# Performance work log

Hardware: AMD Instinct MI355X
Metric: run time of the kernel (lower is better)

## Reference

```python
import jax, jax.numpy as jnp
import numpy as np

ALPHA = 0.01  # LeakyReLU negative slope

def _leaky(x):
    return jnp.where(x > 0, x, ALPHA * x)

def _conv(x, w, b):
    # x: NHWC, w: HWIO, valid padding, stride 1
    return jax.lax.conv_general_dilated(x, w, (1, 1), 'VALID',
        dimension_numbers=('NHWC', 'HWIO', 'NHWC')) + b

def _maxpool2(x):
    return jax.lax.reduce_window(x, -jnp.inf, jax.lax.max,
        (1, 2, 2, 1), (1, 2, 2, 1), 'VALID')

def setup_inputs() -> dict:
    key = jax.random.key(0)
    ks = jax.random.split(key, 32)
    B, S, H = 32, 197, 256
    FLAT = 47 * 62 * 64  # after conv/pool trunk = 186496
    def w(k, shape, fan_in):
        return jax.random.normal(k, shape, dtype=jnp.float32) * np.float32(1.0 / np.sqrt(fan_in))
    inp = {
        'x': jax.random.normal(ks[0], (B, S, H), dtype=jnp.float32),
        'conv1_w': w(ks[1], (3, 3, 1, 32), 9), 'conv1_b': jnp.zeros((32,), jnp.float32),
        'conv2_w': w(ks[2], (3, 3, 32, 64), 288), 'conv2_b': jnp.zeros((64,), jnp.float32),
        'w_c1': w(ks[3], (FLAT, 512), FLAT), 'b_c1': jnp.zeros((512,), jnp.float32),
        'w_c2': w(ks[4], (512, 256), 512), 'b_c2': jnp.zeros((256,), jnp.float32),
        'w_co': w(ks[5], (256, 225 * 13), 256), 'b_co': jnp.zeros((225 * 13,), jnp.float32),
        'w_sm': w(ks[6], (13, 13), 13), 'b_sm': jnp.zeros((13,), jnp.float32),
        'w_r1': w(ks[7], (FLAT, 256), FLAT), 'b_r1': jnp.zeros((256,), jnp.float32),
        'w_r2': w(ks[8], (256, 128), 256), 'b_r2': jnp.zeros((128,), jnp.float32),
        'w_r3': w(ks[9], (128, 128), 128), 'b_r3': jnp.zeros((128,), jnp.float32),
        'w_r4': w(ks[10], (128, 64), 128), 'b_r4': jnp.zeros((64,), jnp.float32),
        'w_ro': w(ks[11], (64, 225 * 4), 64), 'b_ro': jnp.zeros((225 * 4,), jnp.float32),
        'w_sg': w(ks[12], (4, 4), 4), 'b_sg': jnp.zeros((4,), jnp.float32),
    }
    return inp

def reference(x, conv1_w, conv1_b, conv2_w, conv2_b,
              w_c1, b_c1, w_c2, b_c2, w_co, b_co, w_sm, b_sm,
              w_r1, b_r1, w_r2, b_r2, w_r3, b_r3, w_r4, b_r4,
              w_ro, b_ro, w_sg, b_sg):
    # CNN trunk on expanded hidden state (B, S, H, 1)
    h = x[..., None]
    h = jax.nn.relu(_conv(h, conv1_w, conv1_b))
    h = _maxpool2(h)
    h = jax.nn.relu(_conv(h, conv2_w, conv2_b))
    h = _maxpool2(h)
    h = h.reshape(h.shape[0], -1)  # (B, 186496)
    # classification branch (dropout is identity at inference)
    y = _leaky(h @ w_c1 + b_c1)
    y = _leaky(y @ w_c2 + b_c2)
    y = _leaky(y @ w_co + b_co).reshape(-1, 225, 13)
    # 225-step loop of shared Dense(13, softmax) heads -> one batched matmul
    class_out = jax.nn.softmax(jnp.einsum('bpi,ij->bpj', y, w_sm) + b_sm, axis=-1)
    z = _leaky(h @ w_r1 + b_r1)
    z = _leaky(z @ w_r2 + b_r2)
    z = _leaky(z @ w_r3 + b_r3)
    z = _leaky(z @ w_r4 + b_r4)
    z = (z @ w_ro + b_ro).reshape(-1, 225, 4)
    reg_out = jax.nn.sigmoid(jnp.einsum('bpi,ij->bpj', z, w_sg) + b_sg)
    return class_out, reg_out
```

## Files before the change

kernel.cpp:

```cpp
#include <hip/hip_runtime.h>
#include <hip/hip_bf16.h>

#define ALPHA 0.01f

typedef __attribute__((ext_vector_type(8))) __bf16 bf16x8;
typedef __attribute__((ext_vector_type(4))) float f32x4;

#define BATCH 32
#define P1H 97
#define P1W 127
#define P2W 62
#define FLAT 186496
#define GK 768
#define NGK 243
#define PSTRIDE1 16448
#define PSTRIDE2 8256

static __device__ __forceinline__ unsigned short f2bf(float x) {
  union { float f; unsigned u; } c; c.f = x;
  unsigned r = c.u + 0x7fffu + ((c.u >> 16) & 1u);
  return (unsigned short)(r >> 16);
}

__global__ __launch_bounds__(256) void conv1_pool(const float* __restrict__ x,
    const float* __restrict__ w1, const float* __restrict__ b1,
    unsigned short* __restrict__ p1) {
  int pid = blockIdx.x * 256 + threadIdx.x;
  if (pid >= BATCH * P1H * P1W) return;
  int b = pid / (P1H * P1W);
  int rem = pid - b * (P1H * P1W);
  int ph = rem / P1W;
  int pw = rem - ph * P1W;
  const float* xb = x + ((b * 197 + 2 * ph) * 256 + 2 * pw);
  float in[4][4];
#pragma unroll
  for (int r = 0; r < 4; ++r) {
    float2 v0 = *reinterpret_cast<const float2*>(xb + r * 256);
    float2 v1 = *reinterpret_cast<const float2*>(xb + r * 256 + 2);
    in[r][0] = v0.x; in[r][1] = v0.y; in[r][2] = v1.x; in[r][3] = v1.y;
  }
  unsigned pk[16];
#pragma unroll
  for (int c = 0; c < 32; ++c) {
    float s00 = b1[c], s01 = s00, s10 = s00, s11 = s00;
#pragma unroll
    for (int ky = 0; ky < 3; ++ky)
#pragma unroll
      for (int kx = 0; kx < 3; ++kx) {
        float w = w1[(ky * 3 + kx) * 32 + c];
        s00 = fmaf(in[ky][kx], w, s00);
        s01 = fmaf(in[ky][kx + 1], w, s01);
        s10 = fmaf(in[ky + 1][kx], w, s10);
        s11 = fmaf(in[ky + 1][kx + 1], w, s11);
      }
    float m = fmaxf(fmaxf(s00, s01), fmaxf(s10, s11));
    m = fmaxf(m, 0.0f);
    unsigned short u = f2bf(m);
    if (c & 1) pk[c >> 1] |= ((unsigned)u) << 16;
    else pk[c >> 1] = (unsigned)u;
  }
  uint4* dst = reinterpret_cast<uint4*>(p1 + (size_t)pid * 32);
#pragma unroll
  for (int g = 0; g < 4; ++g)
    dst[g] = make_uint4(pk[g * 4], pk[g * 4 + 1], pk[g * 4 + 2], pk[g * 4 + 3]);
}

__global__ __launch_bounds__(256) void repack_w2(const float* __restrict__ w2,
                                                 unsigned short* __restrict__ bpack) {
  int o = blockIdx.x * 256 + threadIdx.x;
  if (o >= 9 * 4 * 512) return;
  int f = o >> 9;
  int within = o & 511;
  int lane = within >> 3, j = within & 7;
  int tap = f >> 2, nf = f & 3;
  int k = ((lane >> 4) << 3) + j;
  int n = nf * 16 + (lane & 15);
  bpack[o] = f2bf(w2[(tap * 32 + k) * 64 + n]);
}

__global__ __launch_bounds__(256) void conv2_pool(const unsigned short* __restrict__ p1,
    const unsigned short* __restrict__ bpack, const float* __restrict__ b2,
    unsigned short* __restrict__ hbf) {
  __shared__ alignas(16) unsigned char lds_buf[65536];
  int prow = blockIdx.x, b = blockIdx.y;
  int tid = threadIdx.x;
  int lane = tid & 63, wid = tid >> 6;
  {
    const uint4* src = reinterpret_cast<const uint4*>(bpack);
    uint4* dst = reinterpret_cast<uint4*>(lds_buf);
    for (int i = tid; i < 2304; i += 256) dst[i] = src[i];
  }
  __syncthreads();
  int row = lane & 15, kg = lane >> 4;
  int rowbase[4];
  int coff[4][3];
#pragma unroll
  for (int mf = 0; mf < 4; ++mf) {
    int m = wid * 64 + mf * 16 + row;
    int cro = m >> 7, cc = m & 127;
    rowbase[mf] = ((b * 97 + 2 * prow + cro) * 127) * 32 + kg * 8;
#pragma unroll
    for (int kx = 0; kx < 3; ++kx) {
      int ic = cc + kx; if (ic > 126) ic = 126;
      coff[mf][kx] = ic * 32;
    }
  }
  f32x4 acc[4][4];
#pragma unroll
  for (int i = 0; i < 4; ++i)
#pragma unroll
    for (int j = 0; j < 4; ++j) acc[i][j] = (f32x4){0.f, 0.f, 0.f, 0.f};

  const bf16x8* bl = reinterpret_cast<const bf16x8*>(lds_buf);
#pragma unroll
  for (int ky = 0; ky < 3; ++ky) {
#pragma unroll
    for (int kx = 0; kx < 3; ++kx) {
      int tap = ky * 3 + kx;
      bf16x8 a[4];
#pragma unroll
      for (int mf = 0; mf < 4; ++mf) {
        int addr = rowbase[mf] + ky * (127 * 32) + coff[mf][kx];
        a[mf] = *reinterpret_cast<const bf16x8*>(p1 + addr);
      }
      bf16x8 bf[4];
#pragma unroll
      for (int nf = 0; nf < 4; ++nf) bf[nf] = bl[(tap * 4 + nf) * 64 + lane];
#pragma unroll
      for (int nf = 0; nf < 4; ++nf)
#pragma unroll
        for (int mf = 0; mf < 4; ++mf)
          acc[mf][nf] = __builtin_amdgcn_mfma_f32_16x16x32_bf16(a[mf], bf[nf], acc[mf][nf], 0, 0, 0);
    }
  }
  __syncthreads();
  float* stage = reinterpret_cast<float*>(lds_buf);
#pragma unroll
  for (int mf = 0; mf < 4; ++mf)
#pragma unroll
    for (int nf = 0; nf < 4; ++nf) {
      int ch = nf * 16 + (lane & 15);
      float bias = b2[ch];
#pragma unroll
      for (int j = 0; j < 4; ++j) {
        int m = wid * 64 + mf * 16 + (lane >> 4) * 4 + j;
        float v = acc[mf][nf][j] + bias;
        stage[m * 64 + ch] = fmaxf(v, 0.f);
      }
    }
  __syncthreads();
  unsigned short* hb = hbf + (size_t)b * FLAT + prow * (P2W * 64);
  for (int o = tid; o < P2W * 64; o += 256) {
    int pw = o >> 6, ch = o & 63;
    int c0 = 2 * pw;
    float v = fmaxf(fmaxf(stage[c0 * 64 + ch], stage[(c0 + 1) * 64 + ch]),
                    fmaxf(stage[(128 + c0) * 64 + ch], stage[(129 + c0) * 64 + ch]));
    hb[o] = f2bf(v);
  }
}

__global__ __launch_bounds__(512) void gemm_mfma(
    const float* __restrict__ w_c1, const float* __restrict__ w_r1,
    const unsigned short* __restrict__ hbf,
    float* __restrict__ part1, float* __restrict__ part2) {
  int kc = blockIdx.x, tile = blockIdx.y;
  int t = threadIdx.x, lane = t & 63, wid = t >> 6;
  int k0 = kc * GK;
  int klen = FLAT - k0; if (klen > GK) klen = GK;
  int nsteps = klen >> 5;
  const float* W; int N, n0;
  if (tile < 2) { W = w_c1; N = 512; n0 = tile * 256; }
  else          { W = w_r1; N = 256; n0 = 0; }
  int cl = lane & 15, kg = lane >> 4;
  const float* Wb0 = W + (size_t)(k0 + kg * 8) * N + (n0 + wid * 32 + cl);
  const float* Wb1 = Wb0 + 16;
  const unsigned short* ha = hbf + (size_t)cl * FLAT + k0 + kg * 8;

  f32x4 acc[2][2];
#pragma unroll
  for (int i = 0; i < 2; ++i)
#pragma unroll
    for (int j = 0; j < 2; ++j) acc[i][j] = (f32x4){0.f, 0.f, 0.f, 0.f};

#pragma unroll 2
  for (int s = 0; s < nsteps; ++s) {
    bf16x8 a0 = *reinterpret_cast<const bf16x8*>(ha + s * 32);
    bf16x8 a1 = *reinterpret_cast<const bf16x8*>(ha + (size_t)16 * FLAT + s * 32);
    const float* wp0 = Wb0 + (size_t)s * 32 * N;
    const float* wp1 = Wb1 + (size_t)s * 32 * N;
    float e0[8], e1[8];
#pragma unroll
    for (int j = 0; j < 8; ++j) {
      e0[j] = wp0[(size_t)j * N];
      e1[j] = wp1[(size_t)j * N];
    }
    union { unsigned u[4]; bf16x8 v; } b0, b1;
#pragma unroll
    for (int p = 0; p < 4; ++p) {
      b0.u[p] = (unsigned)f2bf(e0[2 * p]) | ((unsigned)f2bf(e0[2 * p + 1]) << 16);
      b1.u[p] = (unsigned)f2bf(e1[2 * p]) | ((unsigned)f2bf(e1[2 * p + 1]) << 16);
    }
    acc[0][0] = __builtin_amdgcn_mfma_f32_16x16x32_bf16(a0, b0.v, acc[0][0], 0, 0, 0);
    acc[1][0] = __builtin_amdgcn_mfma_f32_16x16x32_bf16(a1, b0.v, acc[1][0], 0, 0, 0);
    acc[0][1] = __builtin_amdgcn_mfma_f32_16x16x32_bf16(a0, b1.v, acc[0][1], 0, 0, 0);
    acc[1][1] = __builtin_amdgcn_mfma_f32_16x16x32_bf16(a1, b1.v, acc[1][1], 0, 0, 0);
  }

  if (tile < 2) {
    float* out = part1 + (size_t)kc * PSTRIDE1;
#pragma unroll
    for (int mf = 0; mf < 2; ++mf)
#pragma unroll
      for (int nf = 0; nf < 2; ++nf)
#pragma unroll
        for (int j = 0; j < 4; ++j) {
          int m = mf * 16 + kg * 4 + j;
          int n = n0 + wid * 32 + nf * 16 + cl;
          out[m * 512 + n] = acc[mf][nf][j];
        }
  } else {
    float* out = part2 + (size_t)kc * PSTRIDE2;
#pragma unroll
    for (int mf = 0; mf < 2; ++mf)
#pragma unroll
      for (int nf = 0; nf < 2; ++nf)
#pragma unroll
        for (int j = 0; j < 4; ++j) {
          int m = mf * 16 + kg * 4 + j;
          int n = wid * 32 + nf * 16 + cl;
          out[m * 256 + n] = acc[mf][nf][j];
        }
  }
}

__global__ __launch_bounds__(256) void reduce_big(const float* __restrict__ part1,
    const float* __restrict__ part2, const float* __restrict__ b_c1,
    const float* __restrict__ b_r1, float* __restrict__ y1, float* __restrict__ z1) {
  __shared__ float red[8][32];
  int b = blockIdx.x, t = threadIdx.x;
  int oo = t & 31, j = t >> 5;
  float s = 0.f;
  if (b < 512) {
    const float* p = part1 + b * 32 + oo;
    for (int c = j; c < NGK; c += 8) s += p[(size_t)c * PSTRIDE1];
    red[j][oo] = s;
    __syncthreads();
    if (t < 32) {
      float r = 0.f;
#pragma unroll
      for (int jj = 0; jj < 8; ++jj) r += red[jj][t];
      int o = b * 32 + t;
      r += b_c1[o & 511];
      y1[o] = r > 0.f ? r : ALPHA * r;
    }
  } else {
    const float* p = part2 + (b - 512) * 32 + oo;
    for (int c = j; c < NGK; c += 8) s += p[(size_t)c * PSTRIDE2];
    red[j][oo] = s;
    __syncthreads();
    if (t < 32) {
      float r = 0.f;
#pragma unroll
      for (int jj = 0; jj < 8; ++jj) r += red[jj][t];
      int u = (b - 512) * 32 + t;
      r += b_r1[u & 255];
      z1[u] = r > 0.f ? r : ALPHA * r;
    }
  }
}

__global__ __launch_bounds__(256) void tail_all(
    const float* __restrict__ y1g, const float* __restrict__ z1g,
    const float* __restrict__ w_c2, const float* __restrict__ b_c2,
    const float* __restrict__ w_co, const float* __restrict__ b_co,
    const float* __restrict__ w_sm, const float* __restrict__ b_sm,
    const float* __restrict__ w_r2, const float* __restrict__ b_r2,
    const float* __restrict__ w_r3, const float* __restrict__ b_r3,
    const float* __restrict__ w_r4, const float* __restrict__ b_r4,
    const float* __restrict__ w_ro, const float* __restrict__ b_ro,
    const float* __restrict__ w_sg, const float* __restrict__ b_sg,
    float* __restrict__ class_out, float* __restrict__ reg_out) {
  int tile = blockIdx.x, m = blockIdx.y, t = threadIdx.x;
  if (tile < 8) {
    __shared__ float ly1[512], ly2[256], ly3[29 * 13];
    ly1[t] = y1g[m * 512 + t];
    ly1[t + 256] = y1g[m * 512 + 256 + t];
    __syncthreads();
    {
      float s = b_c2[t];
      for (int k = 0; k < 512; ++k) s = fmaf(ly1[k], w_c2[k * 256 + t], s);
      ly2[t] = s > 0.f ? s : ALPHA * s;
    }
    __syncthreads();
    int p0 = tile * 29;
    int np = 225 - p0; if (np > 29) np = 29;
    int ncols = np * 13;
    for (int n = t; n < ncols; n += 256) {
      int col = p0 * 13 + n;
      float s = b_co[col];
      for (int k = 0; k < 256; ++k) s = fmaf(ly2[k], w_co[k * 2925 + col], s);
      ly3[n] = s > 0.f ? s : ALPHA * s;
    }
    __syncthreads();
    if (t < np) {
      float v[13], l[13], mx = -1e30f;
#pragma unroll
      for (int i = 0; i < 13; ++i) v[i] = ly3[t * 13 + i];
#pragma unroll
      for (int j = 0; j < 13; ++j) {
        float s = b_sm[j];
#pragma unroll
        for (int i = 0; i < 13; ++i) s = fmaf(v[i], w_sm[i * 13 + j], s);
        l[j] = s; mx = fmaxf(mx, s);
      }
      float sum = 0.f;
#pragma unroll
      for (int j = 0; j < 13; ++j) { l[j] = expf(l[j] - mx); sum += l[j]; }
      float inv = 1.f / sum;
      float* o = class_out + ((size_t)m * 225 + p0 + t) * 13;
#pragma unroll
      for (int j = 0; j < 13; ++j) o[j] = l[j] * inv;
    }
  } else {
    __shared__ float lz1[256], lz2[128], lz3[128], lz4[64], lzo[57 * 4];
    lz1[t] = z1g[m * 256 + t];
    __syncthreads();
    if (t < 128) {
      float s = b_r2[t];
      for (int k = 0; k < 256; ++k) s = fmaf(lz1[k], w_r2[k * 128 + t], s);
      lz2[t] = s > 0.f ? s : ALPHA * s;
    }
    __syncthreads();
    if (t < 128) {
      float s = b_r3[t];
      for (int k = 0; k < 128; ++k) s = fmaf(lz2[k], w_r3[k * 128 + t], s);
      lz3[t] = s > 0.f ? s : ALPHA * s;
    }
    __syncthreads();
    if (t < 64) {
      float s = b_r4[t];
      for (int k = 0; k < 128; ++k) s = fmaf(lz3[k], w_r4[k * 64 + t], s);
      lz4[t] = s > 0.f ? s : ALPHA * s;
    }
    __syncthreads();
    int p0 = (tile - 8) * 57;
    int np = 225 - p0; if (np > 57) np = 57;
    int ncols = np * 4;
    for (int n = t; n < ncols; n += 256) {
      int col = p0 * 4 + n;
      float s = b_ro[col];
#pragma unroll
      for (int k = 0; k < 64; ++k) s = fmaf(lz4[k], w_ro[k * 900 + col], s);
      lzo[n] = s;
    }
    __syncthreads();
    if (t < np) {
      float z[4];
#pragma unroll
      for (int i = 0; i < 4; ++i) z[i] = lzo[t * 4 + i];
      float* ro = reg_out + ((size_t)m * 225 + p0 + t) * 4;
#pragma unroll
      for (int j = 0; j < 4; ++j) {
        float s = b_sg[j];
#pragma unroll
        for (int i = 0; i < 4; ++i) s = fmaf(z[i], w_sg[i * 4 + j], s);
        ro[j] = 1.f / (1.f + expf(-s));
      }
    }
  }
}

#define OFF_P1     ((size_t)0)
#define OFF_BPACK  ((size_t)25229312)
#define OFF_H      ((size_t)25266176)
#define OFF_PART1  ((size_t)37201920)
#define OFF_PART2  ((size_t)53189376)
#define OFF_Y1     ((size_t)61214208)
#define OFF_Z1     ((size_t)61279744)

extern "C" void kernel_launch(void* const* d_in, const int* in_sizes, int n_in,
                              void* d_out, int out_size, void* d_ws, size_t ws_size,
                              hipStream_t stream) {
  const float* x     = (const float*)d_in[0];
  const float* w1    = (const float*)d_in[1];
  const float* b1    = (const float*)d_in[2];
  const float* w2    = (const float*)d_in[3];
  const float* b2    = (const float*)d_in[4];
  const float* w_c1  = (const float*)d_in[5];
  const float* b_c1  = (const float*)d_in[6];
  const float* w_c2  = (const float*)d_in[7];
  const float* b_c2  = (const float*)d_in[8];
  const float* w_co  = (const float*)d_in[9];
  const float* b_co  = (const float*)d_in[10];
  const float* w_sm  = (const float*)d_in[11];
  const float* b_sm  = (const float*)d_in[12];
  const float* w_r1  = (const float*)d_in[13];
  const float* b_r1  = (const float*)d_in[14];
  const float* w_r2  = (const float*)d_in[15];
  const float* b_r2  = (const float*)d_in[16];
  const float* w_r3  = (const float*)d_in[17];
  const float* b_r3  = (const float*)d_in[18];
  const float* w_r4  = (const float*)d_in[19];
  const float* b_r4  = (const float*)d_in[20];
  const float* w_ro  = (const float*)d_in[21];
  const float* b_ro  = (const float*)d_in[22];
  const float* w_sg  = (const float*)d_in[23];
  const float* b_sg  = (const float*)d_in[24];

  char* ws = (char*)d_ws;
  unsigned short* p1    = (unsigned short*)(ws + OFF_P1);
  unsigned short* bpack = (unsigned short*)(ws + OFF_BPACK);
  unsigned short* hbf   = (unsigned short*)(ws + OFF_H);
  float*          part1 = (float*)(ws + OFF_PART1);
  float*          part2 = (float*)(ws + OFF_PART2);
  float*          y1    = (float*)(ws + OFF_Y1);
  float*          z1    = (float*)(ws + OFF_Z1);

  float* class_out = (float*)d_out;
  float* reg_out   = (float*)d_out + 32 * 225 * 13;

  conv1_pool<<<1540, 256, 0, stream>>>(x, w1, b1, p1);
  repack_w2<<<72, 256, 0, stream>>>(w2, bpack);
  conv2_pool<<<dim3(47, 32), 256, 0, stream>>>(p1, bpack, b2, hbf);
  gemm_mfma<<<dim3(NGK, 3), 512, 0, stream>>>(w_c1, w_r1, hbf, part1, part2);
  reduce_big<<<768, 256, 0, stream>>>(part1, part2, b_c1, b_r1, y1, z1);
  tail_all<<<dim3(12, 32), 256, 0, stream>>>(y1, z1,
      w_c2, b_c2, w_co, b_co, w_sm, b_sm,
      w_r2, b_r2, w_r3, b_r3, w_r4, b_r4,
      w_ro, b_ro, w_sg, b_sg, class_out, reg_out);
}
```

Measured before the change: 261.1 us.

## Stage fp32 weight tiles through double-buffered LDS with coalesced float4 loads

The weight operand of the split-K GEMM was previously read directly from global memory as scattered per-lane scalar loads, eight rows apart. It is now loaded as coalesced float4 rows into a double-buffered shared-memory tile, with the next tile prefetched into registers during the current MFMA step. The intent is to make the weight stream, which dominates memory traffic, fully coalesced and to overlap it with compute. The cost is 64 KB of LDS per block, which limits occupancy, plus two block-wide barriers per k-step.

```diff
diff --git a/kernel.cpp b/kernel.cpp
--- a/kernel.cpp
+++ b/kernel.cpp
@@ -163,6 +163,7 @@
     const float* __restrict__ w_c1, const float* __restrict__ w_r1,
     const unsigned short* __restrict__ hbf,
     float* __restrict__ part1, float* __restrict__ part2) {
+  __shared__ alignas(16) float lw[2][32 * 256];
   int kc = blockIdx.x, tile = blockIdx.y;
   int t = threadIdx.x, lane = t & 63, wid = t >> 6;
   int k0 = kc * GK;
@@ -172,9 +173,20 @@
   if (tile < 2) { W = w_c1; N = 512; n0 = tile * 256; }
   else          { W = w_r1; N = 256; n0 = 0; }
   int cl = lane & 15, kg = lane >> 4;
-  const float* Wb0 = W + (size_t)(k0 + kg * 8) * N + (n0 + wid * 32 + cl);
-  const float* Wb1 = Wb0 + 16;
+
+  const float* wsrc = W + (size_t)(k0 + wid) * N + n0 + (lane << 2);
+  float* ldst = &lw[0][0] + wid * 256 + (lane << 2);
   const unsigned short* ha = hbf + (size_t)cl * FLAT + k0 + kg * 8;
+  int ldsb = (kg * 8) * 256 + wid * 32 + cl;
+
+  float4 st[4];
+#pragma unroll
+  for (int q = 0; q < 4; ++q)
+    st[q] = *reinterpret_cast<const float4*>(wsrc + (size_t)(q * 8) * N);
+#pragma unroll
+  for (int q = 0; q < 4; ++q)
+    *reinterpret_cast<float4*>(ldst + q * 8 * 256) = st[q];
+  __syncthreads();
 
   f32x4 acc[2][2];
 #pragma unroll
@@ -182,17 +194,21 @@
 #pragma unroll
     for (int j = 0; j < 2; ++j) acc[i][j] = (f32x4){0.f, 0.f, 0.f, 0.f};
 
-#pragma unroll 2
-  for (int s = 0; s < nsteps; ++s) {
-    bf16x8 a0 = *reinterpret_cast<const bf16x8*>(ha + s * 32);
-    bf16x8 a1 = *reinterpret_cast<const bf16x8*>(ha + (size_t)16 * FLAT + s * 32);
-    const float* wp0 = Wb0 + (size_t)s * 32 * N;
-    const float* wp1 = Wb1 + (size_t)s * 32 * N;
+  int cur = 0;
+  for (int kt = 0; kt < nsteps; ++kt) {
+    bool pf = (kt + 1 < nsteps);
+    if (pf) {
+#pragma unroll
+      for (int q = 0; q < 4; ++q)
+        st[q] = *reinterpret_cast<const float4*>(
+            wsrc + (size_t)((kt + 1) * 32 + q * 8) * N);
+    }
+    const float* lt = &lw[cur][ldsb];
     float e0[8], e1[8];
 #pragma unroll
     for (int j = 0; j < 8; ++j) {
-      e0[j] = wp0[(size_t)j * N];
-      e1[j] = wp1[(size_t)j * N];
+      e0[j] = lt[j * 256];
+      e1[j] = lt[j * 256 + 16];
     }
     union { unsigned u[4]; bf16x8 v; } b0, b1;
 #pragma unroll
@@ -200,10 +216,21 @@
       b0.u[p] = (unsigned)f2bf(e0[2 * p]) | ((unsigned)f2bf(e0[2 * p + 1]) << 16);
       b1.u[p] = (unsigned)f2bf(e1[2 * p]) | ((unsigned)f2bf(e1[2 * p + 1]) << 16);
     }
+    bf16x8 a0 = *reinterpret_cast<const bf16x8*>(ha + kt * 32);
+    bf16x8 a1 = *reinterpret_cast<const bf16x8*>(ha + (size_t)16 * FLAT + kt * 32);
     acc[0][0] = __builtin_amdgcn_mfma_f32_16x16x32_bf16(a0, b0.v, acc[0][0], 0, 0, 0);
     acc[1][0] = __builtin_amdgcn_mfma_f32_16x16x32_bf16(a1, b0.v, acc[1][0], 0, 0, 0);
     acc[0][1] = __builtin_amdgcn_mfma_f32_16x16x32_bf16(a0, b1.v, acc[0][1], 0, 0, 0);
     acc[1][1] = __builtin_amdgcn_mfma_f32_16x16x32_bf16(a1, b1.v, acc[1][1], 0, 0, 0);
+    if (pf) {
+      __syncthreads();
+      float* dst = &lw[cur ^ 1][0] + wid * 256 + (lane << 2);
+#pragma unroll
+      for (int q = 0; q < 4; ++q)
+        *reinterpret_cast<float4*>(dst + q * 8 * 256) = st[q];
+      __syncthreads();
+      cur ^= 1;
+    }
   }
 
   if (tile < 2) {
```

New measurement: 365.4 us. 39.9% more time.
